# Kernel optimization log

Hardware: AMD Instinct MI355X
Metric: run time of the kernel (lower is better)

Reference implementation:

```python
import jax, jax.numpy as jnp
import numpy as np

B, F, T = 2, 512, 512
D, N, H = 1024, 16, 64   # hidden, heads, head_dim
K = 32                   # time-bias MLP kernal_size
FILT = 4096              # FFN filter size
L = 4                    # num_decoder_blocks
EPS = 1e-6


def _glorot(key, shape, fan_in, fan_out):
    lim = np.sqrt(6.0 / (fan_in + fan_out)).astype(np.float32)
    return jax.random.uniform(key, shape, jnp.float32, -lim, lim)


def setup_inputs() -> dict:
    key = jax.random.key(0)
    ks = jax.random.split(key, 18)
    inp = {
        'decoder_inputs': jax.random.normal(ks[0], (B, F, D), jnp.float32),
        'encoder_outputs': jax.random.normal(ks[1], (B, T, D), jnp.float32),
        'decoder_times_dist': jax.random.uniform(ks[2], (B, F, F), jnp.float32),
        'decoder_encoder_times_dist': jax.random.uniform(ks[3], (B, F, T), jnp.float32),
        'dec_self_attn_bias': jnp.zeros((B, 1, 1, F), jnp.float32),
        'enc_dec_attn_bias': jnp.zeros((B, 1, 1, T), jnp.float32),
        # per-block stacked parameters (leading dim L)
        'Wq': _glorot(ks[4], (L, D, N, H), D, D),
        'Wk': _glorot(ks[5], (L, D, N, H), D, D),
        'Wv': _glorot(ks[6], (L, D, N, H), D, D),
        'Wo': _glorot(ks[7], (L, N, H, D), D, D),
        'Wth': _glorot(ks[8], (L, 1, K), 1, K),
        'bth': jnp.zeros((L, K), jnp.float32),
        'Wto': _glorot(ks[9], (L, K, 1), K, 1),
        'bto': jnp.zeros((L, 1), jnp.float32),
        'Wf1': _glorot(ks[10], (L, D, FILT), D, FILT),
        'bf1': jnp.zeros((L, FILT), jnp.float32),
        'Wf2': _glorot(ks[11], (L, FILT, D), FILT, D),
        'bf2': jnp.zeros((L, D), jnp.float32),
    }
    return inp


def _norm(x):
    # non-trainable LayerNormalization: (x - mean) / (std + eps)
    m = jnp.mean(x, axis=-1, keepdims=True)
    s = jnp.sqrt(jnp.mean((x - m) ** 2, axis=-1, keepdims=True))
    return (x - m) / (s + EPS)


def _attention(x, src, dist, bias, Wq, Wk, Wv, Wo, Wth, bth, Wto, bto):
    q = jnp.einsum('bfd,dnh->bfnh', x, Wq) * (H ** -0.5)
    k = jnp.einsum('btd,dnh->btnh', src, Wk)
    v = jnp.einsum('btd,dnh->btnh', src, Wv)
    # learned time bias: [B,F,T,1] -> relu MLP(K) -> 1 -> [B,F,T]
    hbias = jax.nn.relu(dist[..., None] @ Wth + bth)        # [B,F,T,K]
    qs_bias = (hbias @ Wto + bto)[..., 0]                   # [B,F,T]
    logits = jnp.einsum('btnh,bfnh->bnft', k, q)            # [B,N,F,T]
    logits = logits + bias + qs_bias[:, None]
    w = jax.nn.softmax(logits, axis=-1)
    out = jnp.einsum('bnft,btnh->bfnh', w, v)
    return jnp.einsum('bfnh,nhd->bfd', out, Wo)


def reference(decoder_inputs, encoder_outputs, decoder_times_dist,
              decoder_encoder_times_dist, dec_self_attn_bias, enc_dec_attn_bias,
              Wq, Wk, Wv, Wo, Wth, bth, Wto, bto, Wf1, bf1, Wf2, bf2):
    # decoder_times_dist / dec_self_attn_bias are accepted but unused (as in source call)
    x = decoder_inputs
    for i in range(L):
        # enc-dec attention with pre-norm + residual
        y = _attention(_norm(x), encoder_outputs, decoder_encoder_times_dist,
                       enc_dec_attn_bias, Wq[i], Wk[i], Wv[i], Wo[i],
                       Wth[i], bth[i], Wto[i], bto[i])
        x = x + y
        # FFN with pre-norm + residual
        y = jax.nn.relu(_norm(x) @ Wf1[i] + bf1[i]) @ Wf2[i] + bf2[i]
        x = x + y
    return _norm(x)
```

## Files before the change

kernel.cpp:

```cpp
#include <hip/hip_runtime.h>

typedef unsigned short u16;
typedef __attribute__((ext_vector_type(8))) unsigned short u16x8;
typedef __attribute__((ext_vector_type(4))) unsigned short u16x4;
typedef __attribute__((ext_vector_type(4))) float f32x4;

#define DEVI __device__ __forceinline__

DEVI u16 f2bf(float f){
  unsigned u = __float_as_uint(f);
  u += 0x7FFFu + ((u >> 16) & 1u);
  return (u16)(u >> 16);
}

DEVI void gload16(const void* g, void* l){
  __builtin_amdgcn_global_load_lds((const __attribute__((address_space(1))) void*)g,
                                   (__attribute__((address_space(3))) void*)l, 16, 0, 0);
}

DEVI float wave_sum(float v){
#pragma unroll
  for (int o = 32; o; o >>= 1) v += __shfl_xor(v, o, 64);
  return v;
}

#define MFMA16(a,b,c) __builtin_amdgcn_mfma_f32_16x16x32_bf16((a),(b),(c),0,0,0)

__global__ __launch_bounds__(256) void prep_k(
    const float* __restrict__ Wq, const float* __restrict__ Wk,
    const float* __restrict__ Wv, const float* __restrict__ Wo,
    const float* __restrict__ Wf1, const float* __restrict__ Wf2,
    const float* __restrict__ enc, const float* __restrict__ dist,
    const float* __restrict__ Wth0, const float* __restrict__ bth0,
    const float* __restrict__ Wto0, const float* __restrict__ bto0,
    u16* __restrict__ Wqt, u16* __restrict__ Wkt,
    u16* __restrict__ Wvt, u16* __restrict__ Wot,
    u16* __restrict__ Wf1t, u16* __restrict__ Wf2t,
    u16* __restrict__ encb, float* __restrict__ qs0){
  __shared__ float tile[64][65];
  const int t = blockIdx.x;
  if (t < 12288){
    const float* in; u16* out; int R, C, r0, c0;
    if (t < 4096){
      const int mat = t >> 8, ti = t & 255, sel = mat >> 2, l = mat & 3;
      in  = (sel == 0 ? Wq : sel == 1 ? Wk : sel == 2 ? Wv : Wo) + (size_t)l * 1048576;
      out = (sel == 0 ? Wqt : sel == 1 ? Wkt : sel == 2 ? Wvt : Wot) + (size_t)l * 1048576;
      R = 1024; C = 1024; r0 = (ti >> 4) << 6; c0 = (ti & 15) << 6;
    } else if (t < 8192){
      const int t2 = t - 4096, mat = t2 >> 10, ti = t2 & 1023;
      in = Wf1 + (size_t)mat * 4194304; out = Wf1t + (size_t)mat * 4194304;
      R = 1024; C = 4096; r0 = (ti >> 6) << 6; c0 = (ti & 63) << 6;
    } else {
      const int t2 = t - 8192, mat = t2 >> 10, ti = t2 & 1023;
      in = Wf2 + (size_t)mat * 4194304; out = Wf2t + (size_t)mat * 4194304;
      R = 4096; C = 1024; r0 = (ti >> 4) << 6; c0 = (ti & 15) << 6;
    }
    const int rr0 = threadIdx.x >> 4, cc = (threadIdx.x & 15) * 4;
#pragma unroll
    for (int it = 0; it < 4; it++){
      const int rr = rr0 + it * 16;
      const float4 v = *(const float4*)(in + (size_t)(r0 + rr) * C + c0 + cc);
      tile[rr][cc] = v.x; tile[rr][cc+1] = v.y;
      tile[rr][cc+2] = v.z; tile[rr][cc+3] = v.w;
    }
    __syncthreads();
#pragma unroll
    for (int it = 0; it < 2; it++){
      const int chunk = threadIdx.x + it * 256;
      const int c = chunk >> 3, q = (chunk & 7) * 8;
      union { u16x8 v8; u16 e[8]; } ob;
#pragma unroll
      for (int i = 0; i < 8; i++) ob.e[i] = f2bf(tile[q + i][c]);
      *(u16x8*)(out + (size_t)(c0 + c) * R + r0 + q) = ob.v8;
    }
  } else if (t < 13312){
    const int i = (t - 12288) * 256 + threadIdx.x;
    float4 v = ((const float4*)enc)[i];
    u16x4 o = { f2bf(v.x), f2bf(v.y), f2bf(v.z), f2bf(v.w) };
    ((u16x4*)encb)[i] = o;
  } else {
    const int bi = t - 13312, ly = bi >> 9, xi = bi & 511;
    const float* Wth = Wth0 + ly*32;
    const float* bth = bth0 + ly*32;
    const float* Wto = Wto0 + ly*32;
    float* qs = qs0 + (size_t)ly * 524288;
    const int idx = xi * 256 + threadIdx.x;
    float4 s4 = ((const float4*)dist)[idx];
    float sv[4] = { s4.x, s4.y, s4.z, s4.w };
    float r[4];
    const float b0 = bto0[ly];
#pragma unroll
    for (int c = 0; c < 4; c++) r[c] = b0;
#pragma unroll
    for (int k = 0; k < 32; k++){
      const float wk = Wth[k], bk = bth[k], ok = Wto[k];
#pragma unroll
      for (int c = 0; c < 4; c++){
        float h = fmaxf(sv[c] * wk + bk, 0.0f);
        r[c] += h * ok;
      }
    }
    ((float4*)qs)[idx] = make_float4(r[0], r[1], r[2], r[3]);
  }
}

template<int COPY>
__global__ __launch_bounds__(256) void layernorm_k(const float* __restrict__ in,
                                                   float* __restrict__ x,
                                                   u16* __restrict__ outp){
  const int row = blockIdx.x;
  const int tid = threadIdx.x;
  const float4 v = ((const float4*)(in + (size_t)row * 1024))[tid];
  if (COPY) ((float4*)x)[(size_t)row * 256 + tid] = v;
  __shared__ float sb[8];
  const int wid = tid >> 6, lane = tid & 63;
  float s = wave_sum(v.x + v.y + v.z + v.w);
  if (lane == 0) sb[wid] = s;
  __syncthreads();
  const float mean = (sb[0] + sb[1] + sb[2] + sb[3]) * (1.0f / 1024.0f);
  const float dx = v.x - mean, dy = v.y - mean, dz = v.z - mean, dw = v.w - mean;
  float q = wave_sum(dx*dx + dy*dy + dz*dz + dw*dw);
  if (lane == 0) sb[4 + wid] = q;
  __syncthreads();
  const float sd = sqrtf((sb[4] + sb[5] + sb[6] + sb[7]) * (1.0f / 1024.0f));
  const float inv = 1.0f / (sd + 1e-6f);
  u16x4 o = { f2bf(dx*inv), f2bf(dy*inv), f2bf(dz*inv), f2bf(dw*inv) };
  ((u16x4*)outp)[(size_t)row * 256 + tid] = o;
}

template<int MODE, int BN>
DEVI void gemm128_core(const u16* A, int lda, const u16* Bt, int ldb,
                       int Klen, int Nd, void* Cout,
                       const float* bias, float scale,
                       u16* Als, u16* Bls, int row0, int col0){
  constexpr int WN = BN / 2, FN = BN / 32;
  constexpr int BSZ = BN * 64;
  const int tid = threadIdx.x;
  const int wid = tid >> 6, lane = tid & 63;
  const int wm = wid >> 1, wn = wid & 1;
  const int lrow = lane & 15, g = lane >> 4, e7 = lane & 7;
  f32x4 acc[4][FN] = {};

  const int scol = ((lane & 7) ^ ((lane >> 3) & 7)) * 8;
  const u16* Ag = A + (size_t)(row0 + wid*8 + (lane >> 3)) * lda + scol;
  const u16* Bg = Bt + (size_t)(col0 + wid*8 + (lane >> 3)) * ldb + scol;
  const int dst0 = wid * 512;

  const int nt = Klen >> 6;

#define STAGE128(buf, k0)                                                     \
  {                                                                           \
    _Pragma("unroll")                                                         \
    for (int q = 0; q < 4; q++)                                               \
      gload16(Ag + (size_t)q*32*lda + (k0), Als + (buf)*8192 + dst0 + q*2048);\
    _Pragma("unroll")                                                         \
    for (int q = 0; q < BN/32; q++)                                           \
      gload16(Bg + (size_t)q*32*ldb + (k0), Bls + (buf)*BSZ + dst0 + q*2048); \
  }

  STAGE128(0, 0);
  __syncthreads();

  for (int t = 0; t < nt; t++){
    const int cur = t & 1;
    if (t + 1 < nt) STAGE128(cur ^ 1, (t + 1) << 6);
    const u16* Ab = Als + cur * 8192;
    const u16* Bb = Bls + cur * BSZ;
#pragma unroll
    for (int ks = 0; ks < 2; ks++){
      const int sl = (((ks << 2) + g) ^ e7) << 3;
      u16x8 av[4], bv[FN];
#pragma unroll
      for (int mi = 0; mi < 4; mi++)
        av[mi] = *(const u16x8*)(Ab + (wm*64 + mi*16 + lrow) * 64 + sl);
#pragma unroll
      for (int ni = 0; ni < FN; ni++)
        bv[ni] = *(const u16x8*)(Bb + (wn*WN + ni*16 + lrow) * 64 + sl);
#pragma unroll
      for (int mi = 0; mi < 4; mi++)
#pragma unroll
        for (int ni = 0; ni < FN; ni++)
          acc[mi][ni] = MFMA16(av[mi], bv[ni], acc[mi][ni]);
    }
    __syncthreads();
  }
#undef STAGE128

#pragma unroll
  for (int mi = 0; mi < 4; mi++){
#pragma unroll
    for (int ni = 0; ni < FN; ni++){
      const int col = col0 + wn*WN + ni*16 + lrow;
#pragma unroll
      for (int j = 0; j < 4; j++){
        const int row = row0 + wm*64 + mi*16 + g*4 + j;
        float v = acc[mi][ni][j];
        if (MODE == 3) v = fmaxf(v + bias[col], 0.0f);
        if (MODE == 0 || MODE == 3)
          ((u16*)Cout)[(size_t)row * Nd + col] = f2bf(v);
        else if (MODE == 6)
          ((u16*)Cout)[(size_t)((col >> 9)*16 + (row >> 6)) * 32768
                       + (row & 63) * 512 + (col & 511)] = f2bf(v);
        else
          ((float*)Cout)[(size_t)row * Nd + col] = v;
      }
    }
  }
}

template<int MODE>
__global__ __launch_bounds__(256) void gemm128_k(const u16* __restrict__ A, int lda,
    const u16* __restrict__ Bt, int ldb, int Klen, int Nd, void* __restrict__ Cout,
    const float* __restrict__ bias, float scale){
  __shared__ __align__(16) u16 Als[2 * 8192];
  __shared__ __align__(16) u16 Bls[2 * 4096];
  gemm128_core<MODE, 64>(A, lda, Bt, ldb, Klen, Nd, Cout, bias, scale,
                         Als, Bls, blockIdx.y * 128, blockIdx.x * 64);
}

__global__ __launch_bounds__(256) void gemmKV_k(const u16* __restrict__ encb,
    const u16* __restrict__ Wkt, const u16* __restrict__ Wvt,
    u16* __restrict__ Kb, u16* __restrict__ Vt){
  __shared__ __align__(16) u16 Als[2 * 8192];
  __shared__ __align__(16) u16 Bls[2 * 4096];
  const int z = blockIdx.z, l = z >> 1;
  if ((z & 1) == 0)
    gemm128_core<0, 64>(encb, 1024, Wkt + (size_t)l*1048576, 1024, 1024, 1024,
                        Kb + (size_t)l*1048576, nullptr, 1.0f,
                        Als, Bls, blockIdx.y * 128, blockIdx.x * 64);
  else
    gemm128_core<6, 64>(Wvt + (size_t)l*1048576, 1024, encb, 1024, 1024, 1024,
                        Vt + (size_t)l*1048576, nullptr, 1.0f,
                        Als, Bls, blockIdx.y * 128, blockIdx.x * 64);
}

__global__ __launch_bounds__(256) void gemm_splitk_k(const u16* __restrict__ A, int lda,
    const u16* __restrict__ Bt, int ldb, int Klen, float* __restrict__ part){
  __shared__ __align__(16) u16 Als[2 * 8192];
  __shared__ __align__(16) u16 Bls[2 * 4096];
  const int z = blockIdx.z;
  gemm128_core<5, 64>(A + (size_t)z * Klen, lda, Bt + (size_t)z * Klen, ldb, Klen, 1024,
                      part + (size_t)z * 1048576, nullptr, 1.0f,
                      Als, Bls, blockIdx.y * 128, blockIdx.x * 64);
}

template<int BIAS, int LAST>
__global__ __launch_bounds__(256) void reduce_ln_k(const float* __restrict__ part,
    const float* __restrict__ bias, float* __restrict__ x, u16* __restrict__ xn,
    float* __restrict__ dout){
  const int row = blockIdx.x, tid = threadIdx.x;
  const size_t idx = (size_t)row * 256 + tid;
  float4 v = ((const float4*)x)[idx];
  float4 p0 = ((const float4*)part)[idx];
  float4 p1 = ((const float4*)(part + 1048576))[idx];
  float4 p2 = ((const float4*)(part + 2097152))[idx];
  float4 p3 = ((const float4*)(part + 3145728))[idx];
  v.x += p0.x + p1.x + p2.x + p3.x;
  v.y += p0.y + p1.y + p2.y + p3.y;
  v.z += p0.z + p1.z + p2.z + p3.z;
  v.w += p0.w + p1.w + p2.w + p3.w;
  if (BIAS){
    const float4 b = *(const float4*)(bias + tid * 4);
    v.x += b.x; v.y += b.y; v.z += b.z; v.w += b.w;
  }
  if (!LAST) ((float4*)x)[idx] = v;

  __shared__ float sb[8];
  const int wid = tid >> 6, lane = tid & 63;
  float s = wave_sum(v.x + v.y + v.z + v.w);
  if (lane == 0) sb[wid] = s;
  __syncthreads();
  const float mean = (sb[0] + sb[1] + sb[2] + sb[3]) * (1.0f / 1024.0f);
  const float dx = v.x - mean, dy = v.y - mean, dz = v.z - mean, dw = v.w - mean;
  float q = wave_sum(dx*dx + dy*dy + dz*dz + dw*dw);
  if (lane == 0) sb[4 + wid] = q;
  __syncthreads();
  const float sd = sqrtf((sb[4] + sb[5] + sb[6] + sb[7]) * (1.0f / 1024.0f));
  const float inv = 1.0f / (sd + 1e-6f);
  if (LAST){
    ((float4*)dout)[idx] = make_float4(dx*inv, dy*inv, dz*inv, dw*inv);
  } else {
    u16x4 o = { f2bf(dx*inv), f2bf(dy*inv), f2bf(dz*inv), f2bf(dw*inv) };
    ((u16x4*)xn)[idx] = o;
  }
}

__global__ __launch_bounds__(256, 2) void attn_k(const u16* __restrict__ xn,
    const u16* __restrict__ Wqt,
    const u16* __restrict__ Kb, const u16* __restrict__ Vt,
    const float* __restrict__ qs, const float* __restrict__ abias,
    u16* __restrict__ aout){
  const int n = blockIdx.x, f0 = blockIdx.y * 64, b = blockIdx.z;
  const int w = threadIdx.x >> 6, lane = threadIdx.x & 63;
  const int l15 = lane & 15, g = lane >> 4, e7 = lane & 7;
  const int fw = f0 + w * 16;
  __shared__ __align__(16) u16 Pl[4][16 * 512];
  u16* pw = &Pl[w][0];

  u16x8 qf0, qf1;
  {
    u16* Als = &Pl[0][0];
    u16* Bls = &Pl[1][0];
    const int wm = w >> 1, wn = w & 1;
    f32x4 qac[2][2] = {};
    const int scol = ((lane & 7) ^ ((lane >> 3) & 7)) * 8;
    const u16* Ag = xn + (size_t)(b*512 + f0 + w*8 + (lane >> 3)) * 1024 + scol;
    const u16* Bg = Wqt + (size_t)(n*64 + w*8 + (lane >> 3)) * 1024 + scol;
    const int dq = w * 512;

#define STAGEQ(buf, k0)                                         \
    gload16(Ag + (k0),            Als + (buf)*4096 + dq);       \
    gload16(Ag + 32*1024 + (k0),  Als + (buf)*4096 + dq + 2048);\
    gload16(Bg + (k0),            Bls + (buf)*4096 + dq);       \
    gload16(Bg + 32*1024 + (k0),  Bls + (buf)*4096 + dq + 2048);

    STAGEQ(0, 0);
    __syncthreads();
    for (int t = 0; t < 16; t++){
      const int cur = t & 1;
      if (t < 15){ STAGEQ(cur ^ 1, (t + 1) << 6); }
      const u16* Ab = Als + cur * 4096;
      const u16* Bb = Bls + cur * 4096;
#pragma unroll
      for (int ks = 0; ks < 2; ks++){
        const int sl = (((ks << 2) + g) ^ e7) << 3;
        u16x8 av[2], bv[2];
#pragma unroll
        for (int mi = 0; mi < 2; mi++)
          av[mi] = *(const u16x8*)(Ab + (wm*32 + mi*16 + l15) * 64 + sl);
#pragma unroll
        for (int ni = 0; ni < 2; ni++)
          bv[ni] = *(const u16x8*)(Bb + (wn*32 + ni*16 + l15) * 64 + sl);
#pragma unroll
        for (int mi = 0; mi < 2; mi++)
#pragma unroll
          for (int ni = 0; ni < 2; ni++)
            qac[mi][ni] = MFMA16(av[mi], bv[ni], qac[mi][ni]);
      }
      __syncthreads();
    }
#undef STAGEQ

    u16* Qt = &Pl[2][0];
#pragma unroll
    for (int mi = 0; mi < 2; mi++)
#pragma unroll
      for (int ni = 0; ni < 2; ni++)
#pragma unroll
        for (int j = 0; j < 4; j++){
          const int r = wm*32 + mi*16 + g*4 + j;
          const int c = wn*32 + ni*16 + l15;
          const int byte = r*128 + (((c >> 3) ^ (r & 7)) << 4) + (c & 7)*2;
          *(u16*)((char*)Qt + byte) = f2bf(qac[mi][ni][j] * 0.125f);
        }
    __syncthreads();
    const int r = w*16 + l15;
    const char* qrow = (char*)Qt + r*128;
    qf0 = *(const u16x8*)(qrow + ((g ^ (r & 7)) << 4));
    qf1 = *(const u16x8*)(qrow + (((4 + g) ^ (r & 7)) << 4));
    __syncthreads();
  }

  f32x4 acc[32];
  const u16* kp = Kb + ((size_t)b*512 + l15) * 1024 + n*64 + g*8;
#pragma unroll
  for (int tf = 0; tf < 32; tf++){
    u16x8 k0 = *(const u16x8*)(kp + (size_t)tf*16*1024);
    u16x8 k1 = *(const u16x8*)(kp + (size_t)tf*16*1024 + 32);
    f32x4 z = {0.f, 0.f, 0.f, 0.f};
    z = MFMA16(k0, qf0, z);
    acc[tf] = MFMA16(k1, qf1, z);
  }

  const float* qsp = qs + ((size_t)b*512 + fw + l15) * 512 + g*4;
  const float* abp = abias + (size_t)b*512 + g*4;
  float m = -3.0e38f;
#pragma unroll
  for (int tf = 0; tf < 32; tf++){
    float4 qv = *(const float4*)(qsp + tf*16);
    float4 av = *(const float4*)(abp + tf*16);
    acc[tf][0] += qv.x + av.x;
    acc[tf][1] += qv.y + av.y;
    acc[tf][2] += qv.z + av.z;
    acc[tf][3] += qv.w + av.w;
    m = fmaxf(m, fmaxf(fmaxf(acc[tf][0], acc[tf][1]), fmaxf(acc[tf][2], acc[tf][3])));
  }
  m = fmaxf(m, __shfl_xor(m, 16, 64));
  m = fmaxf(m, __shfl_xor(m, 32, 64));

  float s = 0.f;
#pragma unroll
  for (int tf = 0; tf < 32; tf++){
#pragma unroll
    for (int j = 0; j < 4; j++){
      float e = __expf(acc[tf][j] - m);
      acc[tf][j] = e; s += e;
    }
  }
  s += __shfl_xor(s, 16, 64);
  s += __shfl_xor(s, 32, 64);
  const float inv = 1.0f / s;
  float invj[4];
#pragma unroll
  for (int j = 0; j < 4; j++) invj[j] = __shfl(inv, g*4 + j, 64);

#pragma unroll
  for (int tf = 0; tf < 32; tf++){
    const int chunk = tf*2 + (g >> 1);
    const int boff = (l15 << 10) + ((chunk ^ e7) << 4) + ((g & 1) << 3);
    u16x4 pk = { f2bf(acc[tf][0]), f2bf(acc[tf][1]), f2bf(acc[tf][2]), f2bf(acc[tf][3]) };
    *(u16x4*)((char*)pw + boff) = pk;
  }

  f32x4 oacc[4] = {};
  const u16* vp = Vt + ((size_t)(b*16 + n)*64 + l15) * 512 + g*8;
  for (int kk = 0; kk < 16; kk++){
    u16x8 pa = *(const u16x8*)((char*)pw + (l15 << 10) + ((((kk << 2) + g) ^ e7) << 4));
#pragma unroll
    for (int nf = 0; nf < 4; nf++){
      u16x8 vb = *(const u16x8*)(vp + (size_t)nf*16*512 + kk*32);
      oacc[nf] = MFMA16(pa, vb, oacc[nf]);
    }
  }

  u16* op = aout + ((size_t)b*512 + fw + g*4) * 1024 + n*64 + l15;
#pragma unroll
  for (int nf = 0; nf < 4; nf++)
#pragma unroll
    for (int j = 0; j < 4; j++)
      op[(size_t)j*1024 + nf*16] = f2bf(oacc[nf][j] * invj[j]);
}

extern "C" void kernel_launch(void* const* d_in, const int* in_sizes, int n_in,
                              void* d_out, int out_size, void* d_ws, size_t ws_size,
                              hipStream_t stream){
  const float* dec_in   = (const float*)d_in[0];
  const float* enc      = (const float*)d_in[1];
  const float* dist     = (const float*)d_in[3];
  const float* abias    = (const float*)d_in[5];
  const float* Wq  = (const float*)d_in[6];
  const float* Wk  = (const float*)d_in[7];
  const float* Wv  = (const float*)d_in[8];
  const float* Wo  = (const float*)d_in[9];
  const float* Wth = (const float*)d_in[10];
  const float* bth = (const float*)d_in[11];
  const float* Wto = (const float*)d_in[12];
  const float* bto = (const float*)d_in[13];
  const float* Wf1 = (const float*)d_in[14];
  const float* bf1 = (const float*)d_in[15];
  const float* Wf2 = (const float*)d_in[16];
  const float* bf2 = (const float*)d_in[17];
  float* dout = (float*)d_out;

  char* wp = (char*)d_ws;
  auto alloc = [&](size_t n) -> char* {
    char* p = wp; wp += (n + 255) & ~(size_t)255; return p;
  };
  float* x     = (float*)alloc((size_t)1048576 * 4);
  u16*  xn     = (u16*)alloc((size_t)1048576 * 2);
  u16*  encb   = (u16*)alloc((size_t)1048576 * 2);
  u16*  Wqt    = (u16*)alloc((size_t)4194304 * 2);
  u16*  Wkt    = (u16*)alloc((size_t)4194304 * 2);
  u16*  Wvt    = (u16*)alloc((size_t)4194304 * 2);
  u16*  Wot    = (u16*)alloc((size_t)4194304 * 2);
  u16*  Wf1t   = (u16*)alloc((size_t)16777216 * 2);
  u16*  Wf2t   = (u16*)alloc((size_t)16777216 * 2);
  u16*  Kb     = (u16*)alloc((size_t)4194304 * 2);
  u16*  Vt     = (u16*)alloc((size_t)4194304 * 2);
  float* qs    = (float*)alloc((size_t)2097152 * 4);
  u16*  aout   = (u16*)alloc((size_t)1048576 * 2);
  u16*  ffh    = (u16*)alloc((size_t)4194304 * 2);
  float* part  = (float*)alloc((size_t)4194304 * 4);

  prep_k<<<15360, 256, 0, stream>>>(Wq, Wk, Wv, Wo, Wf1, Wf2, enc, dist,
                                    Wth, bth, Wto, bto,
                                    Wqt, Wkt, Wvt, Wot, Wf1t, Wf2t, encb, qs);
  gemmKV_k<<<dim3(16, 8, 8), 256, 0, stream>>>(encb, Wkt, Wvt, Kb, Vt);
  layernorm_k<1><<<1024, 256, 0, stream>>>(dec_in, x, xn);

  for (int i = 0; i < 4; i++){
    const size_t wo = (size_t)i * 1048576;

    attn_k<<<dim3(16, 8, 2), 256, 0, stream>>>(xn, Wqt + wo, Kb + wo, Vt + wo,
                                               qs + (size_t)i * 524288, abias, aout);

    gemm_splitk_k<<<dim3(16, 8, 4), 256, 0, stream>>>(aout, 1024, Wot + wo, 1024, 256, part);
    reduce_ln_k<0, 0><<<1024, 256, 0, stream>>>(part, nullptr, x, xn, nullptr);

    gemm128_k<3><<<dim3(64, 8), 256, 0, stream>>>(xn, 1024, Wf1t + (size_t)i*4194304, 1024,
                                                  1024, 4096, ffh, bf1 + (size_t)i*4096, 1.0f);
    gemm_splitk_k<<<dim3(16, 8, 4), 256, 0, stream>>>(ffh, 4096, Wf2t + (size_t)i*4194304, 4096,
                                                      1024, part);
    if (i < 3)
      reduce_ln_k<1, 0><<<1024, 256, 0, stream>>>(part, bf2 + (size_t)i*1024, x, xn, nullptr);
    else
      reduce_ln_k<1, 1><<<1024, 256, 0, stream>>>(part, bf2 + (size_t)i*1024, x, nullptr, dout);
  }
}
```

Measured before the change: 459.3 us.

## Consume fp32 weights directly in GEMMs instead of pre-transposing to bf16

Removes the separate prep pass that transposed and converted Wq, Wk, Wo, Wf1 and Wf2 to bf16. A new GEMM core instead loads fp32 weight tiles into registers, converts them to bf16 and writes them transposed and swizzled into LDS, overlapping the global load with the MFMA loop. This avoids writing and rereading about 100 MB of transposed weights. In exchange each GEMM reads fp32 weights, twice the bytes, through plain vector loads rather than direct-to-LDS loads, and does the conversion work inside the hot loop.

```diff
diff --git a/kernel.cpp b/kernel.cpp
--- a/kernel.cpp
+++ b/kernel.cpp
@@ -27,39 +27,23 @@
 #define MFMA16(a,b,c) __builtin_amdgcn_mfma_f32_16x16x32_bf16((a),(b),(c),0,0,0)
 
 __global__ __launch_bounds__(256) void prep_k(
-    const float* __restrict__ Wq, const float* __restrict__ Wk,
-    const float* __restrict__ Wv, const float* __restrict__ Wo,
-    const float* __restrict__ Wf1, const float* __restrict__ Wf2,
-    const float* __restrict__ enc, const float* __restrict__ dist,
+    const float* __restrict__ Wv, const float* __restrict__ enc,
+    const float* __restrict__ dist,
     const float* __restrict__ Wth0, const float* __restrict__ bth0,
     const float* __restrict__ Wto0, const float* __restrict__ bto0,
-    u16* __restrict__ Wqt, u16* __restrict__ Wkt,
-    u16* __restrict__ Wvt, u16* __restrict__ Wot,
-    u16* __restrict__ Wf1t, u16* __restrict__ Wf2t,
-    u16* __restrict__ encb, float* __restrict__ qs0){
+    u16* __restrict__ Wvt, u16* __restrict__ encb, float* __restrict__ qs0){
   __shared__ float tile[64][65];
   const int t = blockIdx.x;
-  if (t < 12288){
-    const float* in; u16* out; int R, C, r0, c0;
-    if (t < 4096){
-      const int mat = t >> 8, ti = t & 255, sel = mat >> 2, l = mat & 3;
-      in  = (sel == 0 ? Wq : sel == 1 ? Wk : sel == 2 ? Wv : Wo) + (size_t)l * 1048576;
-      out = (sel == 0 ? Wqt : sel == 1 ? Wkt : sel == 2 ? Wvt : Wot) + (size_t)l * 1048576;
-      R = 1024; C = 1024; r0 = (ti >> 4) << 6; c0 = (ti & 15) << 6;
-    } else if (t < 8192){
-      const int t2 = t - 4096, mat = t2 >> 10, ti = t2 & 1023;
-      in = Wf1 + (size_t)mat * 4194304; out = Wf1t + (size_t)mat * 4194304;
-      R = 1024; C = 4096; r0 = (ti >> 6) << 6; c0 = (ti & 63) << 6;
-    } else {
-      const int t2 = t - 8192, mat = t2 >> 10, ti = t2 & 1023;
-      in = Wf2 + (size_t)mat * 4194304; out = Wf2t + (size_t)mat * 4194304;
-      R = 4096; C = 1024; r0 = (ti >> 4) << 6; c0 = (ti & 15) << 6;
-    }
+  if (t < 1024){
+    const int mat = t >> 8, ti = t & 255;
+    const float* in = Wv + (size_t)mat * 1048576;
+    u16* out = Wvt + (size_t)mat * 1048576;
+    const int r0 = (ti >> 4) << 6, c0 = (ti & 15) << 6;
     const int rr0 = threadIdx.x >> 4, cc = (threadIdx.x & 15) * 4;
 #pragma unroll
     for (int it = 0; it < 4; it++){
       const int rr = rr0 + it * 16;
-      const float4 v = *(const float4*)(in + (size_t)(r0 + rr) * C + c0 + cc);
+      const float4 v = *(const float4*)(in + (size_t)(r0 + rr) * 1024 + c0 + cc);
       tile[rr][cc] = v.x; tile[rr][cc+1] = v.y;
       tile[rr][cc+2] = v.z; tile[rr][cc+3] = v.w;
     }
@@ -71,15 +55,15 @@
       union { u16x8 v8; u16 e[8]; } ob;
 #pragma unroll
       for (int i = 0; i < 8; i++) ob.e[i] = f2bf(tile[q + i][c]);
-      *(u16x8*)(out + (size_t)(c0 + c) * R + r0 + q) = ob.v8;
-    }
-  } else if (t < 13312){
-    const int i = (t - 12288) * 256 + threadIdx.x;
+      *(u16x8*)(out + (size_t)(c0 + c) * 1024 + r0 + q) = ob.v8;
+    }
+  } else if (t < 2048){
+    const int i = (t - 1024) * 256 + threadIdx.x;
     float4 v = ((const float4*)enc)[i];
     u16x4 o = { f2bf(v.x), f2bf(v.y), f2bf(v.z), f2bf(v.w) };
     ((u16x4*)encb)[i] = o;
   } else {
-    const int bi = t - 13312, ly = bi >> 9, xi = bi & 511;
+    const int bi = t - 2048, ly = bi >> 9, xi = bi & 511;
     const float* Wth = Wth0 + ly*32;
     const float* bth = bth0 + ly*32;
     const float* Wto = Wto0 + ly*32;
@@ -128,10 +112,119 @@
   ((u16x4*)outp)[(size_t)row * 256 + tid] = o;
 }
 
+template<int MODE>
+DEVI void gemmw_core(const u16* A, int lda, const float* W, int ldw,
+                     int kbase, int Klen, int Nd, void* Cout,
+                     const float* bias, u16* Als, u16* Bls, int row0, int col0){
+  const int tid = threadIdx.x;
+  const int wid = tid >> 6, lane = tid & 63;
+  const int wm = wid >> 1, wn = wid & 1;
+  const int lrow = lane & 15, g = lane >> 4, e7 = lane & 7;
+  f32x4 acc[4][2] = {};
+
+  const int scol = ((lane & 7) ^ ((lane >> 3) & 7)) * 8;
+  const u16* Ag = A + (size_t)(row0 + wid*8 + (lane >> 3)) * lda + scol;
+  const int dst0 = wid * 512;
+
+  const int n4 = (tid & 15) * 4, k4 = (tid >> 4) * 4;
+  const float* Wg = W + (size_t)(kbase + k4) * ldw + col0 + n4;
+
+  const int nt = Klen >> 6;
+  float4 wv[4];
+
+#define LOADW(k0)                                                             \
+  { _Pragma("unroll")                                                         \
+    for (int i = 0; i < 4; i++)                                               \
+      wv[i] = *(const float4*)(Wg + (size_t)((k0) + i) * ldw); }
+
+#define WRITEW(buf)                                                           \
+  { const float* vf = (const float*)&wv[0];                                   \
+    _Pragma("unroll")                                                         \
+    for (int no = 0; no < 4; no++){                                           \
+      const int row = n4 + no;                                                \
+      u16x4 o = { f2bf(vf[no]), f2bf(vf[4 + no]),                             \
+                  f2bf(vf[8 + no]), f2bf(vf[12 + no]) };                      \
+      *(u16x4*)(Bls + (buf)*4096 + row*64 +                                   \
+                (((k4 >> 3) ^ (row & 7)) << 3) + (k4 & 7)) = o; } }
+
+#define STAGEA(buf, k0)                                                       \
+  { _Pragma("unroll")                                                         \
+    for (int q = 0; q < 4; q++)                                               \
+      gload16(Ag + (size_t)q*32*lda + (k0), Als + (buf)*8192 + dst0 + q*2048); }
+
+  STAGEA(0, 0); LOADW(0); WRITEW(0);
+  __syncthreads();
+
+  for (int t = 0; t < nt; t++){
+    const int cur = t & 1;
+    if (t + 1 < nt){ STAGEA(cur ^ 1, (t + 1) << 6); LOADW((t + 1) << 6); }
+    const u16* Ab = Als + cur * 8192;
+    const u16* Bb = Bls + cur * 4096;
+#pragma unroll
+    for (int ks = 0; ks < 2; ks++){
+      const int sl = (((ks << 2) + g) ^ e7) << 3;
+      u16x8 av[4], bv[2];
+#pragma unroll
+      for (int mi = 0; mi < 4; mi++)
+        av[mi] = *(const u16x8*)(Ab + (wm*64 + mi*16 + lrow) * 64 + sl);
+#pragma unroll
+      for (int ni = 0; ni < 2; ni++)
+        bv[ni] = *(const u16x8*)(Bb + (wn*32 + ni*16 + lrow) * 64 + sl);
+#pragma unroll
+      for (int mi = 0; mi < 4; mi++)
+#pragma unroll
+        for (int ni = 0; ni < 2; ni++)
+          acc[mi][ni] = MFMA16(av[mi], bv[ni], acc[mi][ni]);
+    }
+    if (t + 1 < nt) WRITEW(cur ^ 1);
+    __syncthreads();
+  }
+#undef LOADW
+#undef WRITEW
+#undef STAGEA
+
+#pragma unroll
+  for (int mi = 0; mi < 4; mi++){
+#pragma unroll
+    for (int ni = 0; ni < 2; ni++){
+      const int col = col0 + wn*32 + ni*16 + lrow;
+#pragma unroll
+      for (int j = 0; j < 4; j++){
+        const int row = row0 + wm*64 + mi*16 + g*4 + j;
+        float v = acc[mi][ni][j];
+        if (MODE == 3) v = fmaxf(v + bias[col], 0.0f);
+        if (MODE == 0 || MODE == 3)
+          ((u16*)Cout)[(size_t)row * Nd + col] = f2bf(v);
+        else
+          ((float*)Cout)[(size_t)row * Nd + col] = v;
+      }
+    }
+  }
+}
+
+template<int MODE>
+__global__ __launch_bounds__(256) void gemmw_k(const u16* __restrict__ A, int lda,
+    const float* __restrict__ W, int ldw, int Klen, int Nd, void* __restrict__ Cout,
+    const float* __restrict__ bias){
+  __shared__ __align__(16) u16 Als[2 * 8192];
+  __shared__ __align__(16) u16 Bls[2 * 4096];
+  gemmw_core<MODE>(A, lda, W, ldw, 0, Klen, Nd, Cout, bias,
+                   Als, Bls, blockIdx.y * 128, blockIdx.x * 64);
+}
+
+__global__ __launch_bounds__(256) void gemmw_splitk_k(const u16* __restrict__ A, int lda,
+    const float* __restrict__ W, int ldw, int Klen, float* __restrict__ part){
+  __shared__ __align__(16) u16 Als[2 * 8192];
+  __shared__ __align__(16) u16 Bls[2 * 4096];
+  const int z = blockIdx.z;
+  gemmw_core<5>(A + (size_t)z * Klen, lda, W, ldw, z * Klen, Klen, 1024,
+                part + (size_t)z * 1048576, nullptr,
+                Als, Bls, blockIdx.y * 128, blockIdx.x * 64);
+}
+
 template<int MODE, int BN>
 DEVI void gemm128_core(const u16* A, int lda, const u16* Bt, int ldb,
                        int Klen, int Nd, void* Cout,
-                       const float* bias, float scale,
                        u16* Als, u16* Bls, int row0, int col0){
   constexpr int WN = BN / 2, FN = BN / 32;
   constexpr int BSZ = BN * 64;
@@ -145,7 +238,6 @@
   const u16* Ag = A + (size_t)(row0 + wid*8 + (lane >> 3)) * lda + scol;
   const u16* Bg = Bt + (size_t)(col0 + wid*8 + (lane >> 3)) * ldb + scol;
   const int dst0 = wid * 512;
-
   const int nt = Klen >> 6;
 
 #define STAGE128(buf, k0)                                                     \
@@ -195,53 +287,30 @@
       for (int j = 0; j < 4; j++){
         const int row = row0 + wm*64 + mi*16 + g*4 + j;
         float v = acc[mi][ni][j];
-        if (MODE == 3) v = fmaxf(v + bias[col], 0.0f);
-        if (MODE == 0 || MODE == 3)
-          ((u16*)Cout)[(size_t)row * Nd + col] = f2bf(v);
-        else if (MODE == 6)
+        if (MODE == 6)
           ((u16*)Cout)[(size_t)((col >> 9)*16 + (row >> 6)) * 32768
                        + (row & 63) * 512 + (col & 511)] = f2bf(v);
         else
-          ((float*)Cout)[(size_t)row * Nd + col] = v;
+          ((u16*)Cout)[(size_t)row * Nd + col] = f2bf(v);
       }
     }
   }
 }
 
-template<int MODE>
-__global__ __launch_bounds__(256) void gemm128_k(const u16* __restrict__ A, int lda,
-    const u16* __restrict__ Bt, int ldb, int Klen, int Nd, void* __restrict__ Cout,
-    const float* __restrict__ bias, float scale){
-  __shared__ __align__(16) u16 Als[2 * 8192];
-  __shared__ __align__(16) u16 Bls[2 * 4096];
-  gemm128_core<MODE, 64>(A, lda, Bt, ldb, Klen, Nd, Cout, bias, scale,
-                         Als, Bls, blockIdx.y * 128, blockIdx.x * 64);
-}
-
 __global__ __launch_bounds__(256) void gemmKV_k(const u16* __restrict__ encb,
-    const u16* __restrict__ Wkt, const u16* __restrict__ Wvt,
+    const float* __restrict__ Wk, const u16* __restrict__ Wvt,
     u16* __restrict__ Kb, u16* __restrict__ Vt){
   __shared__ __align__(16) u16 Als[2 * 8192];
   __shared__ __align__(16) u16 Bls[2 * 4096];
   const int z = blockIdx.z, l = z >> 1;
   if ((z & 1) == 0)
-    gemm128_core<0, 64>(encb, 1024, Wkt + (size_t)l*1048576, 1024, 1024, 1024,
-                        Kb + (size_t)l*1048576, nullptr, 1.0f,
-                        Als, Bls, blockIdx.y * 128, blockIdx.x * 64);
+    gemmw_core<0>(encb, 1024, Wk + (size_t)l*1048576, 1024, 0, 1024, 1024,
+                  Kb + (size_t)l*1048576, nullptr,
+                  Als, Bls, blockIdx.y * 128, blockIdx.x * 64);
   else
     gemm128_core<6, 64>(Wvt + (size_t)l*1048576, 1024, encb, 1024, 1024, 1024,
-                        Vt + (size_t)l*1048576, nullptr, 1.0f,
+                        Vt + (size_t)l*1048576,
                         Als, Bls, blockIdx.y * 128, blockIdx.x * 64);
-}
-
-__global__ __launch_bounds__(256) void gemm_splitk_k(const u16* __restrict__ A, int lda,
-    const u16* __restrict__ Bt, int ldb, int Klen, float* __restrict__ part){
-  __shared__ __align__(16) u16 Als[2 * 8192];
-  __shared__ __align__(16) u16 Bls[2 * 4096];
-  const int z = blockIdx.z;
-  gemm128_core<5, 64>(A + (size_t)z * Klen, lda, Bt + (size_t)z * Klen, ldb, Klen, 1024,
-                      part + (size_t)z * 1048576, nullptr, 1.0f,
-                      Als, Bls, blockIdx.y * 128, blockIdx.x * 64);
 }
 
 template<int BIAS, int LAST>
@@ -286,7 +355,7 @@
 }
 
 __global__ __launch_bounds__(256, 2) void attn_k(const u16* __restrict__ xn,
-    const u16* __restrict__ Wqt,
+    const float* __restrict__ Wq,
     const u16* __restrict__ Kb, const u16* __restrict__ Vt,
     const float* __restrict__ qs, const float* __restrict__ abias,
     u16* __restrict__ aout){
@@ -305,20 +374,34 @@
     f32x4 qac[2][2] = {};
     const int scol = ((lane & 7) ^ ((lane >> 3) & 7)) * 8;
     const u16* Ag = xn + (size_t)(b*512 + f0 + w*8 + (lane >> 3)) * 1024 + scol;
-    const u16* Bg = Wqt + (size_t)(n*64 + w*8 + (lane >> 3)) * 1024 + scol;
     const int dq = w * 512;
-
-#define STAGEQ(buf, k0)                                         \
-    gload16(Ag + (k0),            Als + (buf)*4096 + dq);       \
-    gload16(Ag + 32*1024 + (k0),  Als + (buf)*4096 + dq + 2048);\
-    gload16(Bg + (k0),            Bls + (buf)*4096 + dq);       \
-    gload16(Bg + 32*1024 + (k0),  Bls + (buf)*4096 + dq + 2048);
-
-    STAGEQ(0, 0);
+    const int tid = threadIdx.x;
+    const int n4 = (tid & 15) * 4, k4 = (tid >> 4) * 4;
+    const float* Wg = Wq + (size_t)k4 * 1024 + n*64 + n4;
+    float4 wv[4];
+
+#define QLOADW(k0)                                                  \
+  { _Pragma("unroll")                                               \
+    for (int i = 0; i < 4; i++)                                     \
+      wv[i] = *(const float4*)(Wg + (size_t)((k0) + i) * 1024); }
+#define QWRITEW(buf)                                                \
+  { const float* vf = (const float*)&wv[0];                         \
+    _Pragma("unroll")                                               \
+    for (int no = 0; no < 4; no++){                                 \
+      const int row = n4 + no;                                      \
+      u16x4 o = { f2bf(vf[no]), f2bf(vf[4 + no]),                   \
+                  f2bf(vf[8 + no]), f2bf(vf[12 + no]) };            \
+      *(u16x4*)(Bls + (buf)*4096 + row*64 +                         \
+                (((k4 >> 3) ^ (row & 7)) << 3) + (k4 & 7)) = o; } }
+#define QSTAGEA(buf, k0)                                            \
+    gload16(Ag + (k0),           Als + (buf)*4096 + dq);            \
+    gload16(Ag + 32*1024 + (k0), Als + (buf)*4096 + dq + 2048);
+
+    QSTAGEA(0, 0); QLOADW(0); QWRITEW(0);
     __syncthreads();
     for (int t = 0; t < 16; t++){
       const int cur = t & 1;
-      if (t < 15){ STAGEQ(cur ^ 1, (t + 1) << 6); }
+      if (t < 15){ QSTAGEA(cur ^ 1, (t + 1) << 6); QLOADW((t + 1) << 6); }
       const u16* Ab = Als + cur * 4096;
       const u16* Bb = Bls + cur * 4096;
 #pragma unroll
@@ -337,9 +420,12 @@
           for (int ni = 0; ni < 2; ni++)
             qac[mi][ni] = MFMA16(av[mi], bv[ni], qac[mi][ni]);
       }
+      if (t < 15) QWRITEW(cur ^ 1);
       __syncthreads();
     }
-#undef STAGEQ
+#undef QLOADW
+#undef QWRITEW
+#undef QSTAGEA
 
     u16* Qt = &Pl[2][0];
 #pragma unroll
@@ -459,12 +545,7 @@
   float* x     = (float*)alloc((size_t)1048576 * 4);
   u16*  xn     = (u16*)alloc((size_t)1048576 * 2);
   u16*  encb   = (u16*)alloc((size_t)1048576 * 2);
-  u16*  Wqt    = (u16*)alloc((size_t)4194304 * 2);
-  u16*  Wkt    = (u16*)alloc((size_t)4194304 * 2);
   u16*  Wvt    = (u16*)alloc((size_t)4194304 * 2);
-  u16*  Wot    = (u16*)alloc((size_t)4194304 * 2);
-  u16*  Wf1t   = (u16*)alloc((size_t)16777216 * 2);
-  u16*  Wf2t   = (u16*)alloc((size_t)16777216 * 2);
   u16*  Kb     = (u16*)alloc((size_t)4194304 * 2);
   u16*  Vt     = (u16*)alloc((size_t)4194304 * 2);
   float* qs    = (float*)alloc((size_t)2097152 * 4);
@@ -472,25 +553,23 @@
   u16*  ffh    = (u16*)alloc((size_t)4194304 * 2);
   float* part  = (float*)alloc((size_t)4194304 * 4);
 
-  prep_k<<<15360, 256, 0, stream>>>(Wq, Wk, Wv, Wo, Wf1, Wf2, enc, dist,
-                                    Wth, bth, Wto, bto,
-                                    Wqt, Wkt, Wvt, Wot, Wf1t, Wf2t, encb, qs);
-  gemmKV_k<<<dim3(16, 8, 8), 256, 0, stream>>>(encb, Wkt, Wvt, Kb, Vt);
+  prep_k<<<4096, 256, 0, stream>>>(Wv, enc, dist, Wth, bth, Wto, bto, Wvt, encb, qs);
+  gemmKV_k<<<dim3(16, 8, 8), 256, 0, stream>>>(encb, Wk, Wvt, Kb, Vt);
   layernorm_k<1><<<1024, 256, 0, stream>>>(dec_in, x, xn);
 
   for (int i = 0; i < 4; i++){
     const size_t wo = (size_t)i * 1048576;
 
-    attn_k<<<dim3(16, 8, 2), 256, 0, stream>>>(xn, Wqt + wo, Kb + wo, Vt + wo,
+    attn_k<<<dim3(16, 8, 2), 256, 0, stream>>>(xn, Wq + wo, Kb + wo, Vt + wo,
                                                qs + (size_t)i * 524288, abias, aout);
 
-    gemm_splitk_k<<<dim3(16, 8, 4), 256, 0, stream>>>(aout, 1024, Wot + wo, 1024, 256, part);
+    gemmw_splitk_k<<<dim3(16, 8, 4), 256, 0, stream>>>(aout, 1024, Wo + wo, 1024, 256, part);
     reduce_ln_k<0, 0><<<1024, 256, 0, stream>>>(part, nullptr, x, xn, nullptr);
 
-    gemm128_k<3><<<dim3(64, 8), 256, 0, stream>>>(xn, 1024, Wf1t + (size_t)i*4194304, 1024,
-                                                  1024, 4096, ffh, bf1 + (size_t)i*4096, 1.0f);
-    gemm_splitk_k<<<dim3(16, 8, 4), 256, 0, stream>>>(ffh, 4096, Wf2t + (size_t)i*4194304, 4096,
-                                                      1024, part);
+    gemmw_k<3><<<dim3(64, 8), 256, 0, stream>>>(xn, 1024, Wf1 + (size_t)i*4194304, 4096,
+                                                1024, 4096, ffh, bf1 + (size_t)i*4096);
+    gemmw_splitk_k<<<dim3(16, 8, 4), 256, 0, stream>>>(ffh, 4096, Wf2 + (size_t)i*4194304, 1024,
+                                                       1024, part);
     if (i < 3)
       reduce_ln_k<1, 0><<<1024, 256, 0, stream>>>(part, bf2 + (size_t)i*1024, x, xn, nullptr);
     else
```

New measurement: 555.0 us. +20.8%, slower.
